# Optimization experiments

Hardware: AMD Instinct MI355X
Metric: run time of the kernel (lower is better)

## Reference

```python
import jax, jax.numpy as jnp
import numpy as np

B, C, H, W = 4, 256, 128, 128
HEADS, KD, VD = 8, 64, 64
EPS = 1e-5


def setup_inputs() -> dict:
    key = jax.random.key(0)
    ks = jax.random.split(key, 5)
    s = 0.02
    return {
        "x": jax.random.normal(ks[0], (B, C, H, W), dtype=jnp.float32),
        "wq": jax.random.normal(ks[1], (HEADS * KD, C), dtype=jnp.float32) * s,
        "bq": jnp.zeros((HEADS * KD,), dtype=jnp.float32),
        "wk": jax.random.normal(ks[2], (HEADS * KD, C), dtype=jnp.float32) * s,
        "bk": jnp.zeros((HEADS * KD,), dtype=jnp.float32),
        "wv": jax.random.normal(ks[3], (HEADS * VD, C), dtype=jnp.float32) * s,
        "bv": jnp.zeros((HEADS * VD,), dtype=jnp.float32),
        "wo": jax.random.normal(ks[4], (C, HEADS * VD), dtype=jnp.float32) * s,
        "bo": jnp.zeros((C,), dtype=jnp.float32),
        "g_q": jnp.ones((KD,), dtype=jnp.float32),
        "be_q": jnp.zeros((KD,), dtype=jnp.float32),
        "g_k": jnp.ones((KD,), dtype=jnp.float32),
        "be_k": jnp.zeros((KD,), dtype=jnp.float32),
        "g_v": jnp.ones((VD,), dtype=jnp.float32),
        "be_v": jnp.zeros((VD,), dtype=jnp.float32),
    }


def _conv1x1(t, w, b):
    # t: [B,C,H,W], w: [O,C] -> [B,O,H,W]
    return jnp.einsum("bchw,oc->bohw", t, w) + b[None, :, None, None]


def _ln_dim(t, g, be):
    # LayerNorm over the per-head feature axis (axis=2) of [B,heads,dim,N]
    mu = jnp.mean(t, axis=2, keepdims=True)
    var = jnp.var(t, axis=2, keepdims=True)
    return (t - mu) * jax.lax.rsqrt(var + EPS) * g[None, None, :, None] + be[None, None, :, None]


def reference(x, wq, bq, wk, bk, wv, bv, wo, bo, g_q, be_q, g_k, be_k, g_v, be_v):
    b, c, h, w = x.shape
    n = h * w
    # context defaults to x
    q = _conv1x1(x, wq, bq).reshape(b, HEADS, KD, n)
    k = _conv1x1(x, wk, bk).reshape(b, HEADS, KD, n)
    v = _conv1x1(x, wv, bv).reshape(b, HEADS, VD, n)
    q = _ln_dim(q, g_q, be_q)
    k = _ln_dim(k, g_k, be_k)
    v = _ln_dim(v, g_v, be_v)
    q = jax.nn.softmax(q * (KD ** -0.25), axis=2)  # softmax over key_dim
    k = jax.nn.softmax(k, axis=3)                  # softmax over N
    ctx = jnp.einsum("bhkn,bhvn->bhkv", k, v)      # [B,heads,KD,VD]
    out = jnp.einsum("bhkn,bhkv->bhvn", q, ctx)    # [B,heads,VD,N]
    out = out.reshape(b, HEADS * VD, h, w)
    return _conv1x1(out, wo, bo)
```

## Files before the change

### kernel.cpp

```cpp
#include <hip/hip_runtime.h>
#include <hip/hip_bf16.h>
#include <stdint.h>

typedef unsigned short u16;
typedef __attribute__((__vector_size__(16))) short s16x8;
typedef __attribute__((__vector_size__(16))) float f32x4;

#define N_ 16384
#define C_ 256

__device__ __forceinline__ float bf2f(u16 u) {
    union { uint32_t i; float f; } v; v.i = ((uint32_t)u) << 16; return v.f;
}
__device__ __forceinline__ u16 f2bf(float f) {
    union { uint32_t i; float f; } v; v.f = f;
    uint32_t u = v.i;
    return (u16)((u + 0x7FFFu + ((u >> 16) & 1u)) >> 16);
}

__device__ __forceinline__ void gl_lds16(const u16* g, u16* l) {
    __builtin_amdgcn_global_load_lds((__attribute__((address_space(1))) void*)g,
                                     (__attribute__((address_space(3))) void*)l,
                                     16, 0, 0);
}

__global__ __launch_bounds__(256) void zero_kernel(float* __restrict__ p, int n) {
    int i = blockIdx.x * 256 + threadIdx.x;
    if (i < n) p[i] = 0.f;
}

__global__ __launch_bounds__(256) void transpose_kernel(const float* __restrict__ x,
                                                        u16* __restrict__ xT) {
    __shared__ float T[64][65];
    int tid = threadIdx.x;
    int n0 = blockIdx.x * 64, c0 = blockIdx.y * 64, b = blockIdx.z;
    const float* xp = x + (size_t)b * C_ * N_;
    for (int it = 0; it < 16; it++) {
        int idx = it * 256 + tid;
        int c = idx >> 6, n = idx & 63;
        T[c][n] = xp[(size_t)(c0 + c) * N_ + n0 + n];
    }
    __syncthreads();
    u16* op = xT + (size_t)b * N_ * C_;
    for (int it = 0; it < 8; it++) {
        int idx = it * 256 + tid;
        int n = idx >> 5, c2 = (idx & 31) * 2;
        uint32_t lo = f2bf(T[c2][n]);
        uint32_t hi = f2bf(T[c2 + 1][n]);
        *(uint32_t*)&op[(size_t)(n0 + n) * C_ + c0 + c2] = lo | (hi << 16);
    }
}

__global__ __launch_bounds__(256) void cvtw_kernel(const float* __restrict__ wq,
                                                   const float* __restrict__ wk,
                                                   const float* __restrict__ wv,
                                                   u16* __restrict__ wb) {
    int m = blockIdx.y;
    const float* s = m == 0 ? wq : (m == 1 ? wk : wv);
    int i = blockIdx.x * 256 + threadIdx.x;
    wb[(size_t)m * 131072 + i] = f2bf(s[i]);
}


__global__ __launch_bounds__(256) void kv_kernel(
    const u16* __restrict__ xT, const u16* __restrict__ wb,
    const float* __restrict__ bk, const float* __restrict__ bv,
    const float* __restrict__ gk, const float* __restrict__ bek,
    const float* __restrict__ gv, const float* __restrict__ bev,
    u16* __restrict__ eKb, u16* __restrict__ vbb, float* __restrict__ rs)
{
    __shared__ u16 WS[128 * 64];
    __shared__ u16 XS[128 * 64];
    int tid = threadIdx.x;
    int lane = tid & 63, wid = tid >> 6;
    int quad = lane >> 4, l15 = lane & 15;
    int wm = wid >> 1, wn = wid & 1;
    int bx = blockIdx.x, sec = blockIdx.y, b = blockIdx.z;
    int kind2 = sec >> 2, pair = sec & 3;
    int r0 = pair * 128;
    int n0 = bx * 128;

    const float* bptr  = kind2 ? bv  : bk;
    const float* gptr  = kind2 ? gv  : gk;
    const float* beptr = kind2 ? bev : bek;
    const u16* wsrc = wb + (size_t)(1 + kind2) * 131072 + (size_t)r0 * 256;
    const u16* xsrc = xT + ((size_t)b * N_ + n0) * 256;

    f32x4 acc[4][4];
#pragma unroll
    for (int i = 0; i < 4; i++)
#pragma unroll
        for (int j = 0; j < 4; j++) acc[i][j] = (f32x4){0.f, 0.f, 0.f, 0.f};

    int srow = lane >> 3;
    int sc8  = ((lane & 7) ^ srow) * 8;

    for (int kc = 0; kc < 4; kc++) {
        int koff = kc * 64 + sc8;
#pragma unroll
        for (int i = 0; i < 4; i++) {
            int row = (wid * 4 + i) * 8 + srow;
            gl_lds16(&wsrc[(size_t)row * 256 + koff], &WS[(wid * 4 + i) * 512]);
            gl_lds16(&xsrc[(size_t)row * 256 + koff], &XS[(wid * 4 + i) * 512]);
        }
        __syncthreads();
#pragma unroll
        for (int ks = 0; ks < 2; ks++) {
            int cc = ks * 4 + quad;
            s16x8 af[4], bf[4];
#pragma unroll
            for (int f = 0; f < 4; f++) {
                int ar = wn * 64 + f * 16 + l15;
                int br = wm * 64 + f * 16 + l15;
                af[f] = *(const s16x8*)&XS[ar * 64 + ((cc ^ (ar & 7)) * 8)];
                bf[f] = *(const s16x8*)&WS[br * 64 + ((cc ^ (br & 7)) * 8)];
            }
#pragma unroll
            for (int i = 0; i < 4; i++)
#pragma unroll
                for (int j = 0; j < 4; j++)
                    acc[i][j] = __builtin_amdgcn_mfma_f32_16x16x32_bf16(af[i], bf[j], acc[i][j], 0, 0, 0);
        }
        __syncthreads();
    }

    int head = pair * 2 + wm;
    float bB_[4], gB[4], eB[4];
#pragma unroll
    for (int nf = 0; nf < 4; nf++) {
        int rl = nf * 16 + l15;
        bB_[nf] = bptr[head * 64 + rl];
        gB[nf]  = gptr[rl];
        eB[nf]  = beptr[rl];
    }
#pragma unroll
    for (int mf = 0; mf < 4; mf++)
#pragma unroll
        for (int nf = 0; nf < 4; nf++)
#pragma unroll
            for (int r = 0; r < 4; r++) acc[mf][nf][r] += bB_[nf];
    float sa[4][4], sb[4][4];
#pragma unroll
    for (int mf = 0; mf < 4; mf++)
#pragma unroll
        for (int r = 0; r < 4; r++) {
            float s = 0.f, s2 = 0.f;
#pragma unroll
            for (int nf = 0; nf < 4; nf++) { float v = acc[mf][nf][r]; s += v; s2 += v * v; }
            sa[mf][r] = s; sb[mf][r] = s2;
        }
#pragma unroll
    for (int msk = 1; msk <= 8; msk <<= 1)
#pragma unroll
        for (int mf = 0; mf < 4; mf++)
#pragma unroll
            for (int r = 0; r < 4; r++) {
                sa[mf][r] += __shfl_xor(sa[mf][r], msk);
                sb[mf][r] += __shfl_xor(sb[mf][r], msk);
            }
#pragma unroll
    for (int mf = 0; mf < 4; mf++)
#pragma unroll
        for (int r = 0; r < 4; r++) {
            float mu = sa[mf][r] * (1.f / 64.f);
            float rstd = rsqrtf(sb[mf][r] * (1.f / 64.f) - mu * mu + 1e-5f);
#pragma unroll
            for (int nf = 0; nf < 4; nf++)
                acc[mf][nf][r] = (acc[mf][nf][r] - mu) * rstd * gB[nf] + eB[nf];
        }
    if (kind2 == 0) {
#pragma unroll
        for (int mf = 0; mf < 4; mf++)
#pragma unroll
            for (int nf = 0; nf < 4; nf++)
#pragma unroll
                for (int r = 0; r < 4; r++) acc[mf][nf][r] = __expf(acc[mf][nf][r]);
#pragma unroll
        for (int nf = 0; nf < 4; nf++) {
            float s = 0.f;
#pragma unroll
            for (int mf = 0; mf < 4; mf++)
#pragma unroll
                for (int r = 0; r < 4; r++) s += acc[mf][nf][r];
            s += __shfl_xor(s, 16); s += __shfl_xor(s, 32);
            if (quad == 0)
                atomicAdd(&rs[(size_t)b * 512 + head * 64 + nf * 16 + l15], s);
        }
    }
    u16* op = (kind2 == 0) ? eKb : vbb;
    size_t tb = ((size_t)((b * 8 + head) * 128 + bx)) * 8192;
#pragma unroll
    for (int mf = 0; mf < 4; mf++)
#pragma unroll
        for (int nf = 0; nf < 4; nf++) {
            int rh = nf * 16 + l15;
            int ln = wn * 64 + mf * 16 + quad * 4;
            int c  = ln >> 3;
            int off = rh * 128 + ((c ^ (rh & 15)) * 8) + (ln & 7);
            uint64_t w0 = (uint64_t)f2bf(acc[mf][nf][0]) | ((uint64_t)f2bf(acc[mf][nf][1]) << 16) |
                          ((uint64_t)f2bf(acc[mf][nf][2]) << 32) | ((uint64_t)f2bf(acc[mf][nf][3]) << 48);
            *(uint64_t*)&op[tb + off] = w0;
        }
}

__global__ __launch_bounds__(256) void q_kernel(
    const u16* __restrict__ xT, const u16* __restrict__ wb,
    const float* __restrict__ bq, const float* __restrict__ gq, const float* __restrict__ beq,
    u16* __restrict__ qT)
{
    __shared__ u16 WS[128 * 64];
    __shared__ u16 XS[128 * 64];
    int tid = threadIdx.x;
    int lane = tid & 63, wid = tid >> 6;
    int quad = lane >> 4, l15 = lane & 15;
    int wm = wid >> 1, wn = wid & 1;
    int bx = blockIdx.x, pair = blockIdx.y, b = blockIdx.z;
    int r0 = pair * 128;
    int n0 = bx * 128;

    const u16* wsrc = wb + (size_t)r0 * 256;
    const u16* xsrc = xT + ((size_t)b * N_ + n0) * 256;

    f32x4 acc[4][4];
#pragma unroll
    for (int i = 0; i < 4; i++)
#pragma unroll
        for (int j = 0; j < 4; j++) acc[i][j] = (f32x4){0.f, 0.f, 0.f, 0.f};

    int srow = lane >> 3;
    int sc8  = ((lane & 7) ^ srow) * 8;

    for (int kc = 0; kc < 4; kc++) {
        int koff = kc * 64 + sc8;
#pragma unroll
        for (int i = 0; i < 4; i++) {
            int row = (wid * 4 + i) * 8 + srow;
            gl_lds16(&wsrc[(size_t)row * 256 + koff], &WS[(wid * 4 + i) * 512]);
            gl_lds16(&xsrc[(size_t)row * 256 + koff], &XS[(wid * 4 + i) * 512]);
        }
        __syncthreads();
#pragma unroll
        for (int ks = 0; ks < 2; ks++) {
            int cc = ks * 4 + quad;
            s16x8 af[4], bf[4];
#pragma unroll
            for (int f = 0; f < 4; f++) {
                int ar = wm * 64 + f * 16 + l15;
                int br = wn * 64 + f * 16 + l15;
                af[f] = *(const s16x8*)&WS[ar * 64 + ((cc ^ (ar & 7)) * 8)];
                bf[f] = *(const s16x8*)&XS[br * 64 + ((cc ^ (br & 7)) * 8)];
            }
#pragma unroll
            for (int i = 0; i < 4; i++)
#pragma unroll
                for (int j = 0; j < 4; j++)
                    acc[i][j] = __builtin_amdgcn_mfma_f32_16x16x32_bf16(af[i], bf[j], acc[i][j], 0, 0, 0);
        }
        __syncthreads();
    }

    float bA[4][4], gA[4][4], eA[4][4];
#pragma unroll
    for (int mf = 0; mf < 4; mf++)
#pragma unroll
        for (int r = 0; r < 4; r++) {
            int rl = mf * 16 + quad * 4 + r;
            bA[mf][r] = bq[r0 + wm * 64 + rl];
            gA[mf][r] = gq[rl];
            eA[mf][r] = beq[rl];
        }
#pragma unroll
    for (int mf = 0; mf < 4; mf++)
#pragma unroll
        for (int nf = 0; nf < 4; nf++)
#pragma unroll
            for (int r = 0; r < 4; r++) acc[mf][nf][r] += bA[mf][r];
#pragma unroll
    for (int nf = 0; nf < 4; nf++) {
        float s = 0.f, s2 = 0.f;
#pragma unroll
        for (int mf = 0; mf < 4; mf++)
#pragma unroll
            for (int r = 0; r < 4; r++) { float v = acc[mf][nf][r]; s += v; s2 += v * v; }
        s  += __shfl_xor(s, 16);  s  += __shfl_xor(s, 32);
        s2 += __shfl_xor(s2, 16); s2 += __shfl_xor(s2, 32);
        float mu = s * (1.f / 64.f);
        float rstd = rsqrtf(s2 * (1.f / 64.f) - mu * mu + 1e-5f);
#pragma unroll
        for (int mf = 0; mf < 4; mf++)
#pragma unroll
            for (int r = 0; r < 4; r++)
                acc[mf][nf][r] = (acc[mf][nf][r] - mu) * rstd * gA[mf][r] + eA[mf][r];
    }
    const float s_q = 0.35355339059327373f;
#pragma unroll
    for (int nf = 0; nf < 4; nf++) {
        float m = -1e30f;
#pragma unroll
        for (int mf = 0; mf < 4; mf++)
#pragma unroll
            for (int r = 0; r < 4; r++) { acc[mf][nf][r] *= s_q; m = fmaxf(m, acc[mf][nf][r]); }
        m = fmaxf(m, __shfl_xor(m, 16)); m = fmaxf(m, __shfl_xor(m, 32));
        float d = 0.f;
#pragma unroll
        for (int mf = 0; mf < 4; mf++)
#pragma unroll
            for (int r = 0; r < 4; r++) { float e = __expf(acc[mf][nf][r] - m); acc[mf][nf][r] = e; d += e; }
        d += __shfl_xor(d, 16); d += __shfl_xor(d, 32);
        float inv = 1.f / d;
#pragma unroll
        for (int mf = 0; mf < 4; mf++)
#pragma unroll
            for (int r = 0; r < 4; r++) acc[mf][nf][r] *= inv;
    }
    u16* qp = qT + (size_t)b * N_ * 512;
#pragma unroll
    for (int mf = 0; mf < 4; mf++)
#pragma unroll
        for (int nf = 0; nf < 4; nf++) {
            int n = n0 + wn * 64 + nf * 16 + l15;
            int g0 = r0 + wm * 64 + mf * 16 + quad * 4;
            uint64_t w0 = (uint64_t)f2bf(acc[mf][nf][0]) | ((uint64_t)f2bf(acc[mf][nf][1]) << 16) |
                          ((uint64_t)f2bf(acc[mf][nf][2]) << 32) | ((uint64_t)f2bf(acc[mf][nf][3]) << 48);
            *(uint64_t*)&qp[(size_t)n * 512 + g0] = w0;
        }
}

__global__ __launch_bounds__(256) void ctx_kernel(
    const u16* __restrict__ eKb, const u16* __restrict__ vbb,
    float* __restrict__ ctx_acc)
{
    __shared__ u16 ES[64 * 128];
    __shared__ u16 VS[64 * 128];
    __shared__ float CTXS[64 * 66];
    int tid = threadIdx.x;
    int lane = tid & 63, wid = tid >> 6;
    int quad = lane >> 4, l15 = lane & 15;
    int ns = blockIdx.x, h = blockIdx.y, b = blockIdx.z;
    for (int i = tid; i < 64 * 66; i += 256) CTXS[i] = 0.f;
    size_t hb = (size_t)(b * 8 + h) * 128;
    f32x4 acc[4][4];
#pragma unroll
    for (int i = 0; i < 4; i++)
#pragma unroll
        for (int j = 0; j < 4; j++) acc[i][j] = (f32x4){0.f, 0.f, 0.f, 0.f};

    for (int t = 0; t < 8; t++) {
        size_t tb = (hb + ns * 8 + t) * 8192;
#pragma unroll
        for (int i = 0; i < 4; i++) {
            size_t g = tb + ((size_t)((wid * 4 + i) * 64) + lane) * 8;
            gl_lds16(&eKb[g], &ES[(wid * 4 + i) * 512]);
            gl_lds16(&vbb[g], &VS[(wid * 4 + i) * 512]);
        }
        __syncthreads();
        int cc = wid * 4 + quad;
        s16x8 af[4], bf[4];
#pragma unroll
        for (int f = 0; f < 4; f++) {
            int off = (f * 16 + l15) * 128 + ((cc ^ l15) * 8);
            af[f] = *(const s16x8*)&ES[off];
            bf[f] = *(const s16x8*)&VS[off];
        }
#pragma unroll
        for (int i = 0; i < 4; i++)
#pragma unroll
            for (int j = 0; j < 4; j++)
                acc[i][j] = __builtin_amdgcn_mfma_f32_16x16x32_bf16(af[i], bf[j], acc[i][j], 0, 0, 0);
        __syncthreads();
    }
#pragma unroll
    for (int mf = 0; mf < 4; mf++)
#pragma unroll
        for (int nf = 0; nf < 4; nf++)
#pragma unroll
            for (int r = 0; r < 4; r++) {
                int kd = mf * 16 + quad * 4 + r, vd = nf * 16 + l15;
                atomicAdd(&CTXS[kd * 66 + vd], acc[mf][nf][r]);
            }
    __syncthreads();
    size_t base = ((size_t)b * 8 + h) * 4096;
    for (int i = tid; i < 4096; i += 256)
        atomicAdd(&ctx_acc[base + i], CTXS[(i >> 6) * 66 + (i & 63)]);
}

__global__ __launch_bounds__(256) void weff_kernel(
    const float* __restrict__ ctx_acc, const float* __restrict__ rs,
    const float* __restrict__ wo, u16* __restrict__ Weffb)
{
    __shared__ float CT[16][65];
    int tid = threadIdx.x;
    int h = blockIdx.x, b = blockIdx.y, kc = blockIdx.z;
    for (int i = tid; i < 1024; i += 256) {
        int kdl = i >> 6, vd = i & 63;
        int kd = kc * 16 + kdl;
        CT[kdl][vd] = ctx_acc[(((size_t)b * 8 + h) * 64 + kd) * 64 + vd] /
                      rs[(size_t)b * 512 + h * 64 + kd];
    }
    __syncthreads();
    int c = tid;
    float wrow[64];
    const float4* wp = (const float4*)(wo + (size_t)c * 512 + h * 64);
#pragma unroll
    for (int i = 0; i < 16; i++) { float4 t = wp[i]; wrow[i*4] = t.x; wrow[i*4+1] = t.y; wrow[i*4+2] = t.z; wrow[i*4+3] = t.w; }
    for (int kdl = 0; kdl < 16; kdl++) {
        float s = 0.f;
#pragma unroll
        for (int vd = 0; vd < 64; vd++) s += wrow[vd] * CT[kdl][vd];
        Weffb[((size_t)b * 256 + c) * 512 + h * 64 + kc * 16 + kdl] = f2bf(s);
    }
}

__global__ __launch_bounds__(256) void out_kernel(
    const u16* __restrict__ Weffb, const u16* __restrict__ qT,
    const float* __restrict__ bo, float* __restrict__ out)
{
    __shared__ u16 WS[128 * 64];
    __shared__ u16 XS[128 * 64];
    int tid = threadIdx.x;
    int lane = tid & 63, wid = tid >> 6;
    int quad = lane >> 4, l15 = lane & 15;
    int wm = wid >> 1, wn = wid & 1;
    int n0 = blockIdx.x * 128, c0 = blockIdx.y * 128, b = blockIdx.z;
    const u16* asrc = Weffb + ((size_t)b * 256 + c0) * 512;
    const u16* bsrc = qT + ((size_t)b * N_ + n0) * 512;

    f32x4 acc[4][4];
#pragma unroll
    for (int i = 0; i < 4; i++)
#pragma unroll
        for (int j = 0; j < 4; j++) acc[i][j] = (f32x4){0.f, 0.f, 0.f, 0.f};

    int srow = lane >> 3;
    int sc8  = ((lane & 7) ^ srow) * 8;

    for (int kc = 0; kc < 8; kc++) {
        int koff = kc * 64 + sc8;
#pragma unroll
        for (int i = 0; i < 4; i++) {
            int row = (wid * 4 + i) * 8 + srow;
            gl_lds16(&asrc[(size_t)row * 512 + koff], &WS[(wid * 4 + i) * 512]);
            gl_lds16(&bsrc[(size_t)row * 512 + koff], &XS[(wid * 4 + i) * 512]);
        }
        __syncthreads();
#pragma unroll
        for (int ks = 0; ks < 2; ks++) {
            int cc = ks * 4 + quad;
            s16x8 af[4], bf[4];
#pragma unroll
            for (int f = 0; f < 4; f++) {
                int ar = wm * 64 + f * 16 + l15;
                int br = wn * 64 + f * 16 + l15;
                af[f] = *(const s16x8*)&WS[ar * 64 + ((cc ^ (ar & 7)) * 8)];
                bf[f] = *(const s16x8*)&XS[br * 64 + ((cc ^ (br & 7)) * 8)];
            }
#pragma unroll
            for (int i = 0; i < 4; i++)
#pragma unroll
                for (int j = 0; j < 4; j++)
                    acc[i][j] = __builtin_amdgcn_mfma_f32_16x16x32_bf16(af[i], bf[j], acc[i][j], 0, 0, 0);
        }
        __syncthreads();
    }
#pragma unroll
    for (int mf = 0; mf < 4; mf++)
#pragma unroll
        for (int r = 0; r < 4; r++) {
            int c = c0 + wm * 64 + mf * 16 + quad * 4 + r;
            float bov = bo[c];
#pragma unroll
            for (int nf = 0; nf < 4; nf++)
                out[((size_t)b * 256 + c) * N_ + n0 + wn * 64 + nf * 16 + l15] = acc[mf][nf][r] + bov;
        }
}

extern "C" void kernel_launch(void* const* d_in, const int* in_sizes, int n_in,
                              void* d_out, int out_size, void* d_ws, size_t ws_size,
                              hipStream_t stream) {
    const float* x   = (const float*)d_in[0];
    const float* wq  = (const float*)d_in[1];
    const float* bq  = (const float*)d_in[2];
    const float* wk  = (const float*)d_in[3];
    const float* bk  = (const float*)d_in[4];
    const float* wv  = (const float*)d_in[5];
    const float* bv  = (const float*)d_in[6];
    const float* wo  = (const float*)d_in[7];
    const float* bo  = (const float*)d_in[8];
    const float* gq  = (const float*)d_in[9];
    const float* beq = (const float*)d_in[10];
    const float* gk  = (const float*)d_in[11];
    const float* bek = (const float*)d_in[12];
    const float* gv  = (const float*)d_in[13];
    const float* bev = (const float*)d_in[14];
    float* out = (float*)d_out;

    char* ws = (char*)d_ws;
    u16* xT      = (u16*)(ws);
    u16* wb      = (u16*)(ws + 33554432ULL);
    u16* eKb     = (u16*)(ws + 34340864ULL);
    u16* qT      = (u16*)(ws + 34340864ULL);
    u16* vbb     = (u16*)(ws + 101449728ULL);
    float* ctx_a = (float*)(ws + 168558592ULL);
    float* rs    = (float*)(ws + 169082880ULL);
    u16* Weffb   = (u16*)(ws + 169091072ULL);

    cvtw_kernel<<<dim3(512, 3), 256, 0, stream>>>(wq, wk, wv, wb);
    transpose_kernel<<<dim3(256, 4, 4), 256, 0, stream>>>(x, xT);
    zero_kernel<<<dim3(520), 256, 0, stream>>>(ctx_a, 133120);

    kv_kernel<<<dim3(128, 8, 4), 256, 0, stream>>>(
        xT, wb, bk, bv, gk, bek, gv, bev, eKb, vbb, rs);

    ctx_kernel<<<dim3(16, 8, 4), 256, 0, stream>>>(eKb, vbb, ctx_a);

    q_kernel<<<dim3(128, 4, 4), 256, 0, stream>>>(xT, wb, bq, gq, beq, qT);

    weff_kernel<<<dim3(8, 4, 4), 256, 0, stream>>>(ctx_a, rs, wo, Weffb);

    out_kernel<<<dim3(128, 2, 4), 256, 0, stream>>>(Weffb, qT, bo, out);
}
```

Baseline: 382.1 us.

## Fuse K/V projection with context reduction and Q projection with output GEMM

K and V projections are computed per 128-column tile in one block, kept in LDS, and reduced into the per-head context with atomic accumulation. This removes the eK/V bf16 intermediates and the separate ctx kernel. The Q projection with its layernorm and softmax is also fused into the output GEMM, so the 128-column Q tile per pair never round-trips through global memory. The cost is more LDS per block (64KB), more atomics on ctx, and the Weff operand read straight from global memory inside the inner loop.

Measured after the change: 435.6 us. 14.0% more time.

```diff
diff --git a/kernel.cpp b/kernel.cpp
--- a/kernel.cpp
+++ b/kernel.cpp
@@ -9,9 +9,6 @@
 #define N_ 16384
 #define C_ 256
 
-__device__ __forceinline__ float bf2f(u16 u) {
-    union { uint32_t i; float f; } v; v.i = ((uint32_t)u) << 16; return v.f;
-}
 __device__ __forceinline__ u16 f2bf(float f) {
     union { uint32_t i; float f; } v; v.f = f;
     uint32_t u = v.i;
@@ -61,327 +58,181 @@
     wb[(size_t)m * 131072 + i] = f2bf(s[i]);
 }
 
-
-__global__ __launch_bounds__(256) void kv_kernel(
+__global__ __launch_bounds__(256) void kv_ctx_kernel(
     const u16* __restrict__ xT, const u16* __restrict__ wb,
     const float* __restrict__ bk, const float* __restrict__ bv,
     const float* __restrict__ gk, const float* __restrict__ bek,
     const float* __restrict__ gv, const float* __restrict__ bev,
-    u16* __restrict__ eKb, u16* __restrict__ vbb, float* __restrict__ rs)
+    float* __restrict__ ctx_acc, float* __restrict__ rs)
 {
-    __shared__ u16 WS[128 * 64];
-    __shared__ u16 XS[128 * 64];
-    int tid = threadIdx.x;
-    int lane = tid & 63, wid = tid >> 6;
-    int quad = lane >> 4, l15 = lane & 15;
-    int wm = wid >> 1, wn = wid & 1;
-    int bx = blockIdx.x, sec = blockIdx.y, b = blockIdx.z;
-    int kind2 = sec >> 2, pair = sec & 3;
-    int r0 = pair * 128;
-    int n0 = bx * 128;
-
-    const float* bptr  = kind2 ? bv  : bk;
-    const float* gptr  = kind2 ? gv  : gk;
-    const float* beptr = kind2 ? bev : bek;
-    const u16* wsrc = wb + (size_t)(1 + kind2) * 131072 + (size_t)r0 * 256;
-    const u16* xsrc = xT + ((size_t)b * N_ + n0) * 256;
-
-    f32x4 acc[4][4];
-#pragma unroll
-    for (int i = 0; i < 4; i++)
-#pragma unroll
-        for (int j = 0; j < 4; j++) acc[i][j] = (f32x4){0.f, 0.f, 0.f, 0.f};
-
-    int srow = lane >> 3;
-    int sc8  = ((lane & 7) ^ srow) * 8;
-
-    for (int kc = 0; kc < 4; kc++) {
-        int koff = kc * 64 + sc8;
-#pragma unroll
-        for (int i = 0; i < 4; i++) {
-            int row = (wid * 4 + i) * 8 + srow;
-            gl_lds16(&wsrc[(size_t)row * 256 + koff], &WS[(wid * 4 + i) * 512]);
-            gl_lds16(&xsrc[(size_t)row * 256 + koff], &XS[(wid * 4 + i) * 512]);
-        }
-        __syncthreads();
-#pragma unroll
-        for (int ks = 0; ks < 2; ks++) {
-            int cc = ks * 4 + quad;
-            s16x8 af[4], bf[4];
-#pragma unroll
-            for (int f = 0; f < 4; f++) {
-                int ar = wn * 64 + f * 16 + l15;
-                int br = wm * 64 + f * 16 + l15;
-                af[f] = *(const s16x8*)&XS[ar * 64 + ((cc ^ (ar & 7)) * 8)];
-                bf[f] = *(const s16x8*)&WS[br * 64 + ((cc ^ (br & 7)) * 8)];
-            }
-#pragma unroll
-            for (int i = 0; i < 4; i++)
-#pragma unroll
-                for (int j = 0; j < 4; j++)
-                    acc[i][j] = __builtin_amdgcn_mfma_f32_16x16x32_bf16(af[i], bf[j], acc[i][j], 0, 0, 0);
-        }
-        __syncthreads();
-    }
-
-    int head = pair * 2 + wm;
-    float bB_[4], gB[4], eB[4];
-#pragma unroll
-    for (int nf = 0; nf < 4; nf++) {
-        int rl = nf * 16 + l15;
-        bB_[nf] = bptr[head * 64 + rl];
-        gB[nf]  = gptr[rl];
-        eB[nf]  = beptr[rl];
-    }
-#pragma unroll
-    for (int mf = 0; mf < 4; mf++)
-#pragma unroll
-        for (int nf = 0; nf < 4; nf++)
-#pragma unroll
-            for (int r = 0; r < 4; r++) acc[mf][nf][r] += bB_[nf];
-    float sa[4][4], sb[4][4];
-#pragma unroll
-    for (int mf = 0; mf < 4; mf++)
-#pragma unroll
-        for (int r = 0; r < 4; r++) {
-            float s = 0.f, s2 = 0.f;
-#pragma unroll
-            for (int nf = 0; nf < 4; nf++) { float v = acc[mf][nf][r]; s += v; s2 += v * v; }
-            sa[mf][r] = s; sb[mf][r] = s2;
-        }
-#pragma unroll
-    for (int msk = 1; msk <= 8; msk <<= 1)
-#pragma unroll
-        for (int mf = 0; mf < 4; mf++)
-#pragma unroll
-            for (int r = 0; r < 4; r++) {
-                sa[mf][r] += __shfl_xor(sa[mf][r], msk);
-                sb[mf][r] += __shfl_xor(sb[mf][r], msk);
-            }
-#pragma unroll
-    for (int mf = 0; mf < 4; mf++)
-#pragma unroll
-        for (int r = 0; r < 4; r++) {
-            float mu = sa[mf][r] * (1.f / 64.f);
-            float rstd = rsqrtf(sb[mf][r] * (1.f / 64.f) - mu * mu + 1e-5f);
-#pragma unroll
-            for (int nf = 0; nf < 4; nf++)
-                acc[mf][nf][r] = (acc[mf][nf][r] - mu) * rstd * gB[nf] + eB[nf];
-        }
-    if (kind2 == 0) {
-#pragma unroll
-        for (int mf = 0; mf < 4; mf++)
-#pragma unroll
-            for (int nf = 0; nf < 4; nf++)
-#pragma unroll
-                for (int r = 0; r < 4; r++) acc[mf][nf][r] = __expf(acc[mf][nf][r]);
-#pragma unroll
-        for (int nf = 0; nf < 4; nf++) {
-            float s = 0.f;
-#pragma unroll
-            for (int mf = 0; mf < 4; mf++)
-#pragma unroll
-                for (int r = 0; r < 4; r++) s += acc[mf][nf][r];
-            s += __shfl_xor(s, 16); s += __shfl_xor(s, 32);
-            if (quad == 0)
-                atomicAdd(&rs[(size_t)b * 512 + head * 64 + nf * 16 + l15], s);
-        }
-    }
-    u16* op = (kind2 == 0) ? eKb : vbb;
-    size_t tb = ((size_t)((b * 8 + head) * 128 + bx)) * 8192;
-#pragma unroll
-    for (int mf = 0; mf < 4; mf++)
-#pragma unroll
-        for (int nf = 0; nf < 4; nf++) {
-            int rh = nf * 16 + l15;
-            int ln = wn * 64 + mf * 16 + quad * 4;
-            int c  = ln >> 3;
-            int off = rh * 128 + ((c ^ (rh & 15)) * 8) + (ln & 7);
-            uint64_t w0 = (uint64_t)f2bf(acc[mf][nf][0]) | ((uint64_t)f2bf(acc[mf][nf][1]) << 16) |
-                          ((uint64_t)f2bf(acc[mf][nf][2]) << 32) | ((uint64_t)f2bf(acc[mf][nf][3]) << 48);
-            *(uint64_t*)&op[tb + off] = w0;
-        }
-}
-
-__global__ __launch_bounds__(256) void q_kernel(
-    const u16* __restrict__ xT, const u16* __restrict__ wb,
-    const float* __restrict__ bq, const float* __restrict__ gq, const float* __restrict__ beq,
-    u16* __restrict__ qT)
-{
-    __shared__ u16 WS[128 * 64];
-    __shared__ u16 XS[128 * 64];
+    __shared__ u16 LDSU[32768];
+    u16* WS = LDSU;
+    u16* XS = LDSU + 8192;
+    u16* VT = LDSU + 16384;
+    u16* ET = LDSU;
+
     int tid = threadIdx.x;
     int lane = tid & 63, wid = tid >> 6;
     int quad = lane >> 4, l15 = lane & 15;
     int wm = wid >> 1, wn = wid & 1;
     int bx = blockIdx.x, pair = blockIdx.y, b = blockIdx.z;
-    int r0 = pair * 128;
     int n0 = bx * 128;
-
-    const u16* wsrc = wb + (size_t)r0 * 256;
+    int head = pair * 2 + wm;
+
     const u16* xsrc = xT + ((size_t)b * N_ + n0) * 256;
-
-    f32x4 acc[4][4];
-#pragma unroll
-    for (int i = 0; i < 4; i++)
-#pragma unroll
-        for (int j = 0; j < 4; j++) acc[i][j] = (f32x4){0.f, 0.f, 0.f, 0.f};
-
     int srow = lane >> 3;
     int sc8  = ((lane & 7) ^ srow) * 8;
 
-    for (int kc = 0; kc < 4; kc++) {
-        int koff = kc * 64 + sc8;
-#pragma unroll
-        for (int i = 0; i < 4; i++) {
-            int row = (wid * 4 + i) * 8 + srow;
-            gl_lds16(&wsrc[(size_t)row * 256 + koff], &WS[(wid * 4 + i) * 512]);
-            gl_lds16(&xsrc[(size_t)row * 256 + koff], &XS[(wid * 4 + i) * 512]);
-        }
-        __syncthreads();
-#pragma unroll
-        for (int ks = 0; ks < 2; ks++) {
-            int cc = ks * 4 + quad;
-            s16x8 af[4], bf[4];
-#pragma unroll
-            for (int f = 0; f < 4; f++) {
-                int ar = wm * 64 + f * 16 + l15;
-                int br = wn * 64 + f * 16 + l15;
-                af[f] = *(const s16x8*)&WS[ar * 64 + ((cc ^ (ar & 7)) * 8)];
-                bf[f] = *(const s16x8*)&XS[br * 64 + ((cc ^ (br & 7)) * 8)];
-            }
-#pragma unroll
-            for (int i = 0; i < 4; i++)
-#pragma unroll
-                for (int j = 0; j < 4; j++)
-                    acc[i][j] = __builtin_amdgcn_mfma_f32_16x16x32_bf16(af[i], bf[j], acc[i][j], 0, 0, 0);
-        }
-        __syncthreads();
-    }
-
-    float bA[4][4], gA[4][4], eA[4][4];
+    for (int kind = 0; kind < 2; kind++) {
+        const u16* wsrc = wb + (size_t)(2 - kind) * 131072 + (size_t)pair * 128 * 256;
+        const float* bptr  = kind ? bk  : bv;
+        const float* gptr  = kind ? gk  : gv;
+        const float* beptr = kind ? bek : bev;
+
+        f32x4 acc[4][4];
+#pragma unroll
+        for (int i = 0; i < 4; i++)
+#pragma unroll
+            for (int j = 0; j < 4; j++) acc[i][j] = (f32x4){0.f, 0.f, 0.f, 0.f};
+
+        for (int kc = 0; kc < 4; kc++) {
+            int koff = kc * 64 + sc8;
+#pragma unroll
+            for (int i = 0; i < 4; i++) {
+                int rg = wid * 4 + i;
+                gl_lds16(&wsrc[(size_t)(rg * 8 + srow) * 256 + koff], &WS[rg * 512]);
+                gl_lds16(&xsrc[(size_t)(rg * 8 + srow) * 256 + koff], &XS[rg * 512]);
+            }
+            __syncthreads();
+#pragma unroll
+            for (int ks = 0; ks < 2; ks++) {
+                int cc = ks * 4 + quad;
+                s16x8 af[4], bf[4];
+#pragma unroll
+                for (int f = 0; f < 4; f++) {
+                    int ar = wn * 64 + f * 16 + l15;
+                    int br = wm * 64 + f * 16 + l15;
+                    af[f] = *(const s16x8*)&XS[ar * 64 + ((cc ^ (ar & 7)) * 8)];
+                    bf[f] = *(const s16x8*)&WS[br * 64 + ((cc ^ (br & 7)) * 8)];
+                }
+#pragma unroll
+                for (int i = 0; i < 4; i++)
+#pragma unroll
+                    for (int j = 0; j < 4; j++)
+                        acc[i][j] = __builtin_amdgcn_mfma_f32_16x16x32_bf16(af[i], bf[j], acc[i][j], 0, 0, 0);
+            }
+            __syncthreads();
+        }
+
+        float bB_[4], gB[4], eB[4];
+#pragma unroll
+        for (int nf = 0; nf < 4; nf++) {
+            int rl = nf * 16 + l15;
+            bB_[nf] = bptr[head * 64 + rl];
+            gB[nf]  = gptr[rl];
+            eB[nf]  = beptr[rl];
+        }
+#pragma unroll
+        for (int mf = 0; mf < 4; mf++)
+#pragma unroll
+            for (int nf = 0; nf < 4; nf++)
+#pragma unroll
+                for (int r = 0; r < 4; r++) acc[mf][nf][r] += bB_[nf];
+        float sa[4][4], sb[4][4];
+#pragma unroll
+        for (int mf = 0; mf < 4; mf++)
+#pragma unroll
+            for (int r = 0; r < 4; r++) {
+                float s = 0.f, s2 = 0.f;
+#pragma unroll
+                for (int nf = 0; nf < 4; nf++) { float v = acc[mf][nf][r]; s += v; s2 += v * v; }
+                sa[mf][r] = s; sb[mf][r] = s2;
+            }
+#pragma unroll
+        for (int msk = 1; msk <= 8; msk <<= 1)
+#pragma unroll
+            for (int mf = 0; mf < 4; mf++)
+#pragma unroll
+                for (int r = 0; r < 4; r++) {
+                    sa[mf][r] += __shfl_xor(sa[mf][r], msk);
+                    sb[mf][r] += __shfl_xor(sb[mf][r], msk);
+                }
+#pragma unroll
+        for (int mf = 0; mf < 4; mf++)
+#pragma unroll
+            for (int r = 0; r < 4; r++) {
+                float mu = sa[mf][r] * (1.f / 64.f);
+                float rstd = rsqrtf(sb[mf][r] * (1.f / 64.f) - mu * mu + 1e-5f);
+#pragma unroll
+                for (int nf = 0; nf < 4; nf++)
+                    acc[mf][nf][r] = (acc[mf][nf][r] - mu) * rstd * gB[nf] + eB[nf];
+            }
+        if (kind == 1) {
+#pragma unroll
+            for (int mf = 0; mf < 4; mf++)
+#pragma unroll
+                for (int nf = 0; nf < 4; nf++)
+#pragma unroll
+                    for (int r = 0; r < 4; r++) acc[mf][nf][r] = __expf(acc[mf][nf][r]);
+#pragma unroll
+            for (int nf = 0; nf < 4; nf++) {
+                float s = 0.f;
+#pragma unroll
+                for (int mf = 0; mf < 4; mf++)
+#pragma unroll
+                    for (int r = 0; r < 4; r++) s += acc[mf][nf][r];
+                s += __shfl_xor(s, 16); s += __shfl_xor(s, 32);
+                if (quad == 0)
+                    atomicAdd(&rs[(size_t)b * 512 + head * 64 + nf * 16 + l15], s);
+            }
+        }
+        u16* dst = kind ? ET : VT;
+#pragma unroll
+        for (int mf = 0; mf < 4; mf++)
+#pragma unroll
+            for (int nf = 0; nf < 4; nf++) {
+                int rh = wm * 64 + nf * 16 + l15;
+                int ln = wn * 64 + mf * 16 + quad * 4;
+                int c  = ln >> 3;
+                int off = rh * 128 + ((c ^ (rh & 15)) * 8) + (ln & 7);
+                uint64_t w0 = (uint64_t)f2bf(acc[mf][nf][0]) | ((uint64_t)f2bf(acc[mf][nf][1]) << 16) |
+                              ((uint64_t)f2bf(acc[mf][nf][2]) << 32) | ((uint64_t)f2bf(acc[mf][nf][3]) << 48);
+                *(uint64_t*)&dst[off] = w0;
+            }
+    }
+    __syncthreads();
+
+    int hh = wid >> 1, kh = wid & 1;
+    f32x4 accc[4][4];
+#pragma unroll
+    for (int i = 0; i < 4; i++)
+#pragma unroll
+        for (int j = 0; j < 4; j++) accc[i][j] = (f32x4){0.f, 0.f, 0.f, 0.f};
+#pragma unroll
+    for (int ks = 0; ks < 2; ks++) {
+        int cc = kh * 8 + ks * 4 + quad;
+        s16x8 af[4], bf[4];
+#pragma unroll
+        for (int f = 0; f < 4; f++) {
+            int off = (hh * 64 + f * 16 + l15) * 128 + ((cc ^ l15) * 8);
+            af[f] = *(const s16x8*)&ET[off];
+            bf[f] = *(const s16x8*)&VT[off];
+        }
+#pragma unroll
+        for (int i = 0; i < 4; i++)
+#pragma unroll
+            for (int j = 0; j < 4; j++)
+                accc[i][j] = __builtin_amdgcn_mfma_f32_16x16x32_bf16(af[i], bf[j], accc[i][j], 0, 0, 0);
+    }
+    size_t base = (size_t)(b * 8 + pair * 2 + hh) * 4096;
 #pragma unroll
     for (int mf = 0; mf < 4; mf++)
 #pragma unroll
-        for (int r = 0; r < 4; r++) {
-            int rl = mf * 16 + quad * 4 + r;
-            bA[mf][r] = bq[r0 + wm * 64 + rl];
-            gA[mf][r] = gq[rl];
-            eA[mf][r] = beq[rl];
-        }
-#pragma unroll
-    for (int mf = 0; mf < 4; mf++)
-#pragma unroll
         for (int nf = 0; nf < 4; nf++)
 #pragma unroll
-            for (int r = 0; r < 4; r++) acc[mf][nf][r] += bA[mf][r];
-#pragma unroll
-    for (int nf = 0; nf < 4; nf++) {
-        float s = 0.f, s2 = 0.f;
-#pragma unroll
-        for (int mf = 0; mf < 4; mf++)
-#pragma unroll
-            for (int r = 0; r < 4; r++) { float v = acc[mf][nf][r]; s += v; s2 += v * v; }
-        s  += __shfl_xor(s, 16);  s  += __shfl_xor(s, 32);
-        s2 += __shfl_xor(s2, 16); s2 += __shfl_xor(s2, 32);
-        float mu = s * (1.f / 64.f);
-        float rstd = rsqrtf(s2 * (1.f / 64.f) - mu * mu + 1e-5f);
-#pragma unroll
-        for (int mf = 0; mf < 4; mf++)
-#pragma unroll
             for (int r = 0; r < 4; r++)
-                acc[mf][nf][r] = (acc[mf][nf][r] - mu) * rstd * gA[mf][r] + eA[mf][r];
-    }
-    const float s_q = 0.35355339059327373f;
-#pragma unroll
-    for (int nf = 0; nf < 4; nf++) {
-        float m = -1e30f;
-#pragma unroll
-        for (int mf = 0; mf < 4; mf++)
-#pragma unroll
-            for (int r = 0; r < 4; r++) { acc[mf][nf][r] *= s_q; m = fmaxf(m, acc[mf][nf][r]); }
-        m = fmaxf(m, __shfl_xor(m, 16)); m = fmaxf(m, __shfl_xor(m, 32));
-        float d = 0.f;
-#pragma unroll
-        for (int mf = 0; mf < 4; mf++)
-#pragma unroll
-            for (int r = 0; r < 4; r++) { float e = __expf(acc[mf][nf][r] - m); acc[mf][nf][r] = e; d += e; }
-        d += __shfl_xor(d, 16); d += __shfl_xor(d, 32);
-        float inv = 1.f / d;
-#pragma unroll
-        for (int mf = 0; mf < 4; mf++)
-#pragma unroll
-            for (int r = 0; r < 4; r++) acc[mf][nf][r] *= inv;
-    }
-    u16* qp = qT + (size_t)b * N_ * 512;
-#pragma unroll
-    for (int mf = 0; mf < 4; mf++)
-#pragma unroll
-        for (int nf = 0; nf < 4; nf++) {
-            int n = n0 + wn * 64 + nf * 16 + l15;
-            int g0 = r0 + wm * 64 + mf * 16 + quad * 4;
-            uint64_t w0 = (uint64_t)f2bf(acc[mf][nf][0]) | ((uint64_t)f2bf(acc[mf][nf][1]) << 16) |
-                          ((uint64_t)f2bf(acc[mf][nf][2]) << 32) | ((uint64_t)f2bf(acc[mf][nf][3]) << 48);
-            *(uint64_t*)&qp[(size_t)n * 512 + g0] = w0;
-        }
-}
-
-__global__ __launch_bounds__(256) void ctx_kernel(
-    const u16* __restrict__ eKb, const u16* __restrict__ vbb,
-    float* __restrict__ ctx_acc)
-{
-    __shared__ u16 ES[64 * 128];
-    __shared__ u16 VS[64 * 128];
-    __shared__ float CTXS[64 * 66];
-    int tid = threadIdx.x;
-    int lane = tid & 63, wid = tid >> 6;
-    int quad = lane >> 4, l15 = lane & 15;
-    int ns = blockIdx.x, h = blockIdx.y, b = blockIdx.z;
-    for (int i = tid; i < 64 * 66; i += 256) CTXS[i] = 0.f;
-    size_t hb = (size_t)(b * 8 + h) * 128;
-    f32x4 acc[4][4];
-#pragma unroll
-    for (int i = 0; i < 4; i++)
-#pragma unroll
-        for (int j = 0; j < 4; j++) acc[i][j] = (f32x4){0.f, 0.f, 0.f, 0.f};
-
-    for (int t = 0; t < 8; t++) {
-        size_t tb = (hb + ns * 8 + t) * 8192;
-#pragma unroll
-        for (int i = 0; i < 4; i++) {
-            size_t g = tb + ((size_t)((wid * 4 + i) * 64) + lane) * 8;
-            gl_lds16(&eKb[g], &ES[(wid * 4 + i) * 512]);
-            gl_lds16(&vbb[g], &VS[(wid * 4 + i) * 512]);
-        }
-        __syncthreads();
-        int cc = wid * 4 + quad;
-        s16x8 af[4], bf[4];
-#pragma unroll
-        for (int f = 0; f < 4; f++) {
-            int off = (f * 16 + l15) * 128 + ((cc ^ l15) * 8);
-            af[f] = *(const s16x8*)&ES[off];
-            bf[f] = *(const s16x8*)&VS[off];
-        }
-#pragma unroll
-        for (int i = 0; i < 4; i++)
-#pragma unroll
-            for (int j = 0; j < 4; j++)
-                acc[i][j] = __builtin_amdgcn_mfma_f32_16x16x32_bf16(af[i], bf[j], acc[i][j], 0, 0, 0);
-        __syncthreads();
-    }
-#pragma unroll
-    for (int mf = 0; mf < 4; mf++)
-#pragma unroll
-        for (int nf = 0; nf < 4; nf++)
-#pragma unroll
-            for (int r = 0; r < 4; r++) {
-                int kd = mf * 16 + quad * 4 + r, vd = nf * 16 + l15;
-                atomicAdd(&CTXS[kd * 66 + vd], acc[mf][nf][r]);
-            }
-    __syncthreads();
-    size_t base = ((size_t)b * 8 + h) * 4096;
-    for (int i = tid; i < 4096; i += 256)
-        atomicAdd(&ctx_acc[base + i], CTXS[(i >> 6) * 66 + (i & 63)]);
+                atomicAdd(&ctx_acc[base + (size_t)(mf * 16 + quad * 4 + r) * 64 + nf * 16 + l15],
+                          accc[mf][nf][r]);
 }
 
 __global__ __launch_bounds__(256) void weff_kernel(
@@ -411,66 +262,167 @@
     }
 }
 
-__global__ __launch_bounds__(256) void out_kernel(
-    const u16* __restrict__ Weffb, const u16* __restrict__ qT,
-    const float* __restrict__ bo, float* __restrict__ out)
+__global__ __launch_bounds__(256) void q_out_kernel(
+    const u16* __restrict__ xT, const u16* __restrict__ wb,
+    const float* __restrict__ bq, const float* __restrict__ gq, const float* __restrict__ beq,
+    const u16* __restrict__ Weffb, const float* __restrict__ bo, float* __restrict__ out)
 {
-    __shared__ u16 WS[128 * 64];
-    __shared__ u16 XS[128 * 64];
+    __shared__ u16 WS[8192];
+    __shared__ u16 XS[4096];
+    __shared__ u16 PT[8192];
     int tid = threadIdx.x;
     int lane = tid & 63, wid = tid >> 6;
     int quad = lane >> 4, l15 = lane & 15;
     int wm = wid >> 1, wn = wid & 1;
-    int n0 = blockIdx.x * 128, c0 = blockIdx.y * 128, b = blockIdx.z;
-    const u16* asrc = Weffb + ((size_t)b * 256 + c0) * 512;
-    const u16* bsrc = qT + ((size_t)b * N_ + n0) * 512;
-
-    f32x4 acc[4][4];
-#pragma unroll
-    for (int i = 0; i < 4; i++)
-#pragma unroll
-        for (int j = 0; j < 4; j++) acc[i][j] = (f32x4){0.f, 0.f, 0.f, 0.f};
-
+    int bx = blockIdx.x, b = blockIdx.y;
+    int n0 = bx * 64;
+
+    const u16* xsrc = xT + ((size_t)b * N_ + n0) * 256;
     int srow = lane >> 3;
     int sc8  = ((lane & 7) ^ srow) * 8;
 
-    for (int kc = 0; kc < 8; kc++) {
-        int koff = kc * 64 + sc8;
-#pragma unroll
-        for (int i = 0; i < 4; i++) {
-            int row = (wid * 4 + i) * 8 + srow;
-            gl_lds16(&asrc[(size_t)row * 512 + koff], &WS[(wid * 4 + i) * 512]);
-            gl_lds16(&bsrc[(size_t)row * 512 + koff], &XS[(wid * 4 + i) * 512]);
-        }
+    f32x4 acco[4][4];
+#pragma unroll
+    for (int i = 0; i < 4; i++)
+#pragma unroll
+        for (int j = 0; j < 4; j++) acco[i][j] = (f32x4){0.f, 0.f, 0.f, 0.f};
+
+    for (int pair = 0; pair < 4; pair++) {
+        const u16* wsrc = wb + (size_t)pair * 128 * 256;
+        f32x4 acc[4][2];
+#pragma unroll
+        for (int i = 0; i < 4; i++)
+#pragma unroll
+            for (int j = 0; j < 2; j++) acc[i][j] = (f32x4){0.f, 0.f, 0.f, 0.f};
+
+        for (int kc = 0; kc < 4; kc++) {
+            int koff = kc * 64 + sc8;
+#pragma unroll
+            for (int i = 0; i < 4; i++) {
+                int rg = wid * 4 + i;
+                gl_lds16(&wsrc[(size_t)(rg * 8 + srow) * 256 + koff], &WS[rg * 512]);
+            }
+#pragma unroll
+            for (int i = 0; i < 2; i++) {
+                int rg = wid * 2 + i;
+                gl_lds16(&xsrc[(size_t)(rg * 8 + srow) * 256 + koff], &XS[rg * 512]);
+            }
+            __syncthreads();
+#pragma unroll
+            for (int ks = 0; ks < 2; ks++) {
+                int cc = ks * 4 + quad;
+                s16x8 af[4], bf[2];
+#pragma unroll
+                for (int f = 0; f < 4; f++) {
+                    int ar = wm * 64 + f * 16 + l15;
+                    af[f] = *(const s16x8*)&WS[ar * 64 + ((cc ^ (ar & 7)) * 8)];
+                }
+#pragma unroll
+                for (int f = 0; f < 2; f++) {
+                    int br = wn * 32 + f * 16 + l15;
+                    bf[f] = *(const s16x8*)&XS[br * 64 + ((cc ^ (br & 7)) * 8)];
+                }
+#pragma unroll
+                for (int i = 0; i < 4; i++)
+#pragma unroll
+                    for (int j = 0; j < 2; j++)
+                        acc[i][j] = __builtin_amdgcn_mfma_f32_16x16x32_bf16(af[i], bf[j], acc[i][j], 0, 0, 0);
+            }
+            __syncthreads();
+        }
+
+#pragma unroll
+        for (int mf = 0; mf < 4; mf++)
+#pragma unroll
+            for (int r = 0; r < 4; r++) {
+                int rl = mf * 16 + quad * 4 + r;
+                float bb = bq[pair * 128 + wm * 64 + rl];
+#pragma unroll
+                for (int nf = 0; nf < 2; nf++) acc[mf][nf][r] += bb;
+            }
+#pragma unroll
+        for (int nf = 0; nf < 2; nf++) {
+            float s = 0.f, s2 = 0.f;
+#pragma unroll
+            for (int mf = 0; mf < 4; mf++)
+#pragma unroll
+                for (int r = 0; r < 4; r++) { float v = acc[mf][nf][r]; s += v; s2 += v * v; }
+            s  += __shfl_xor(s, 16);  s  += __shfl_xor(s, 32);
+            s2 += __shfl_xor(s2, 16); s2 += __shfl_xor(s2, 32);
+            float mu = s * (1.f / 64.f);
+            float rstd = rsqrtf(s2 * (1.f / 64.f) - mu * mu + 1e-5f);
+#pragma unroll
+            for (int mf = 0; mf < 4; mf++)
+#pragma unroll
+                for (int r = 0; r < 4; r++) {
+                    int rl = mf * 16 + quad * 4 + r;
+                    acc[mf][nf][r] = (acc[mf][nf][r] - mu) * rstd * gq[rl] + beq[rl];
+                }
+        }
+        const float s_q = 0.35355339059327373f;
+#pragma unroll
+        for (int nf = 0; nf < 2; nf++) {
+            float m = -1e30f;
+#pragma unroll
+            for (int mf = 0; mf < 4; mf++)
+#pragma unroll
+                for (int r = 0; r < 4; r++) { acc[mf][nf][r] *= s_q; m = fmaxf(m, acc[mf][nf][r]); }
+            m = fmaxf(m, __shfl_xor(m, 16)); m = fmaxf(m, __shfl_xor(m, 32));
+            float d = 0.f;
+#pragma unroll
+            for (int mf = 0; mf < 4; mf++)
+#pragma unroll
+                for (int r = 0; r < 4; r++) { float e = __expf(acc[mf][nf][r] - m); acc[mf][nf][r] = e; d += e; }
+            d += __shfl_xor(d, 16); d += __shfl_xor(d, 32);
+            float inv = 1.f / d;
+#pragma unroll
+            for (int mf = 0; mf < 4; mf++)
+#pragma unroll
+                for (int r = 0; r < 4; r++) acc[mf][nf][r] *= inv;
+        }
+#pragma unroll
+        for (int mf = 0; mf < 4; mf++)
+#pragma unroll
+            for (int nf = 0; nf < 2; nf++) {
+                int nl = wn * 32 + nf * 16 + l15;
+                int rl = wm * 64 + mf * 16 + quad * 4;
+                int c  = rl >> 3;
+                int off = nl * 128 + ((c ^ (nl & 15)) * 8) + (rl & 7);
+                uint64_t w0 = (uint64_t)f2bf(acc[mf][nf][0]) | ((uint64_t)f2bf(acc[mf][nf][1]) << 16) |
+                              ((uint64_t)f2bf(acc[mf][nf][2]) << 32) | ((uint64_t)f2bf(acc[mf][nf][3]) << 48);
+                *(uint64_t*)&PT[off] = w0;
+            }
         __syncthreads();
-#pragma unroll
-        for (int ks = 0; ks < 2; ks++) {
+
+#pragma unroll
+        for (int ks = 0; ks < 4; ks++) {
             int cc = ks * 4 + quad;
             s16x8 af[4], bf[4];
 #pragma unroll
-            for (int f = 0; f < 4; f++) {
-                int ar = wm * 64 + f * 16 + l15;
-                int br = wn * 64 + f * 16 + l15;
-                af[f] = *(const s16x8*)&WS[ar * 64 + ((cc ^ (ar & 7)) * 8)];
-                bf[f] = *(const s16x8*)&XS[br * 64 + ((cc ^ (br & 7)) * 8)];
-            }
+            for (int f = 0; f < 4; f++)
+                af[f] = *(const s16x8*)&Weffb[((size_t)(b * 256 + wid * 64 + f * 16 + l15)) * 512 +
+                                              pair * 128 + cc * 8];
+#pragma unroll
+            for (int f = 0; f < 4; f++)
+                bf[f] = *(const s16x8*)&PT[(f * 16 + l15) * 128 + ((cc ^ l15) * 8)];
 #pragma unroll
             for (int i = 0; i < 4; i++)
 #pragma unroll
                 for (int j = 0; j < 4; j++)
-                    acc[i][j] = __builtin_amdgcn_mfma_f32_16x16x32_bf16(af[i], bf[j], acc[i][j], 0, 0, 0);
+                    acco[i][j] = __builtin_amdgcn_mfma_f32_16x16x32_bf16(af[i], bf[j], acco[i][j], 0, 0, 0);
         }
         __syncthreads();
     }
+
 #pragma unroll
     for (int mf = 0; mf < 4; mf++)
 #pragma unroll
         for (int r = 0; r < 4; r++) {
-            int c = c0 + wm * 64 + mf * 16 + quad * 4 + r;
-            float bov = bo[c];
+            int c = wid * 64 + mf * 16 + quad * 4 + r;
+            float bb = bo[c];
 #pragma unroll
             for (int nf = 0; nf < 4; nf++)
-                out[((size_t)b * 256 + c) * N_ + n0 + wn * 64 + nf * 16 + l15] = acc[mf][nf][r] + bov;
+                out[((size_t)(b * 256 + c)) * N_ + n0 + nf * 16 + l15] = acco[mf][nf][r] + bb;
         }
 }
 
@@ -497,25 +449,19 @@
     char* ws = (char*)d_ws;
     u16* xT      = (u16*)(ws);
     u16* wb      = (u16*)(ws + 33554432ULL);
-    u16* eKb     = (u16*)(ws + 34340864ULL);
-    u16* qT      = (u16*)(ws + 34340864ULL);
-    u16* vbb     = (u16*)(ws + 101449728ULL);
-    float* ctx_a = (float*)(ws + 168558592ULL);
-    float* rs    = (float*)(ws + 169082880ULL);
-    u16* Weffb   = (u16*)(ws + 169091072ULL);
+    float* ctx_a = (float*)(ws + 34340864ULL);
+    float* rs    = (float*)(ws + 34865152ULL);
+    u16* Weffb   = (u16*)(ws + 34873344ULL);
 
     cvtw_kernel<<<dim3(512, 3), 256, 0, stream>>>(wq, wk, wv, wb);
     transpose_kernel<<<dim3(256, 4, 4), 256, 0, stream>>>(x, xT);
     zero_kernel<<<dim3(520), 256, 0, stream>>>(ctx_a, 133120);
 
-    kv_kernel<<<dim3(128, 8, 4), 256, 0, stream>>>(
-        xT, wb, bk, bv, gk, bek, gv, bev, eKb, vbb, rs);
-
-    ctx_kernel<<<dim3(16, 8, 4), 256, 0, stream>>>(eKb, vbb, ctx_a);
-
-    q_kernel<<<dim3(128, 4, 4), 256, 0, stream>>>(xT, wb, bq, gq, beq, qT);
+    kv_ctx_kernel<<<dim3(128, 4, 4), 256, 0, stream>>>(
+        xT, wb, bk, bv, gk, bek, gv, bev, ctx_a, rs);
 
     weff_kernel<<<dim3(8, 4, 4), 256, 0, stream>>>(ctx_a, rs, wo, Weffb);
 
-    out_kernel<<<dim3(128, 2, 4), 256, 0, stream>>>(Weffb, qT, bo, out);
-}
+    q_out_kernel<<<dim3(256, 4), 256, 0, stream>>>(
+        xT, wb, bq, gq, beq, Weffb, bo, out);
+}
```
